# Performance work log

Measured on AMD Instinct MI355X. Metric: run time of the kernel, lower is better.

Reference implementation:

```python
import jax, jax.numpy as jnp
import numpy as np


def setup_inputs() -> dict:
    key = jax.random.key(0)
    k0, k1, k2, k3, k4 = jax.random.split(key, 5)
    dim, b, h, w = 256, 32, 56, 56
    x = jax.random.normal(k0, (b, dim, h, w), jnp.float32)
    # 1x1 conv qk: weight [out=dim, in=dim], bias [dim]
    qk_w = jax.random.normal(k1, (dim, dim), jnp.float32) * (1.0 / np.sqrt(dim))
    qk_b = jax.random.normal(k2, (dim,), jnp.float32) * 0.01
    # depthwise 3x3 conv pe: weight [dim, 1, 3, 3], bias [dim]
    pe_w = jax.random.normal(k3, (dim, 1, 3, 3), jnp.float32) * (1.0 / 3.0)
    pe_b = jax.random.normal(k4, (dim,), jnp.float32) * 0.01
    return {"x": x, "qk_w": qk_w, "qk_b": qk_b, "pe_w": pe_w, "pe_b": pe_b}


def reference(x, qk_w, qk_b, pe_w, pe_b):
    b, c, h, w = x.shape
    n = h * w
    d = c // 2                      # head_dim = dim // 2
    s = float(n) ** -0.5
    # 1x1 conv + (elu + 1) feature map
    qk = jnp.einsum('bchw,oc->bohw', x, qk_w) + qk_b[None, :, None, None]
    qk = jax.nn.elu(qk) + 1.0
    qk = qk.reshape(b, 2, d, n)
    q, k = qk[:, 0], qk[:, 1]       # each [b, d, n]
    v = x.reshape(b, c, n)          # [b, c, n]
    # kv outer product: (k*s) @ (v^T * s) -> [b, d, c]
    kv = jnp.einsum('bdn,bcn->bdc', k, v) * (s * s)
    # numerator q^T @ kv -> [b, n, c]
    num = jnp.einsum('bdn,bdc->bnc', q, kv)
    # denominator q^T @ mean(k, axis=-1) -> [b, n, 1]
    den = jnp.einsum('bdn,bd->bn', q, jnp.mean(k, axis=-1))[:, :, None] + 1e-6
    attn = (num / den).transpose(0, 2, 1).reshape(b, c, h, w)
    # depthwise 3x3 positional conv on v (= x)
    pe = jax.lax.conv_general_dilated(
        x, pe_w, window_strides=(1, 1), padding='SAME',
        dimension_numbers=('NCHW', 'OIHW', 'NCHW'), feature_group_count=c)
    return attn + pe + pe_b[None, :, None, None]
```

## Files before the change

### kernel.cpp

```cpp
#include <hip/hip_runtime.h>

#define B_ 32
#define C_ 256
#define D_ 128
#define HH 56
#define WW 56
#define N_ 3136
#define KSPLIT 14
#define KRANGE 224

typedef float f32x4 __attribute__((ext_vector_type(4)));
typedef short s16x8 __attribute__((ext_vector_type(8)));
typedef unsigned short u16x8 __attribute__((ext_vector_type(8)));

__device__ __forceinline__ int swz4(int r){
  return (r & 3) ^ (((r >> 2) & 1) << 1) ^ ((r >> 3) & 1);
}
__device__ __forceinline__ unsigned short f2bf(float f){
  unsigned u = __float_as_uint(f);
  u += 0x7fffu + ((u >> 16) & 1u);
  return (unsigned short)(u >> 16);
}
__device__ __forceinline__ float bf2f(unsigned short h){
  return __uint_as_float(((unsigned)h) << 16);
}
__device__ __forceinline__ float elu1(float v){
  return v > 0.f ? v + 1.f : __expf(v);
}
__device__ __forceinline__ unsigned cvtpk(float lo, float hi){
  unsigned r;
  asm("v_cvt_pk_bf16_f32 %0, %1, %2" : "=v"(r) : "v"(lo), "v"(hi));
  return r;
}

template<int R>
__device__ __forceinline__ void stage_glds(const unsigned short* gp, int ld, char* lds){
  const int tid = threadIdx.x;
  const int wid = tid >> 6;
#pragma unroll
  for (int q = 0; q < R/64; ++q){
    const int slot = q*256 + tid;
    const int r = slot >> 2, gi = slot & 3;
    const int u = gi ^ swz4(r);
    const unsigned short* ga = gp + r*ld + u*8;
    char* lb = lds + (q*256 + wid*64)*16;
    __builtin_amdgcn_global_load_lds(
        (__attribute__((address_space(1))) void*)ga,
        (__attribute__((address_space(3))) void*)lb, 16, 0, 0);
  }
}

__device__ __forceinline__ s16x8 ldsfrag(const char* lds, int r, int g){
  return *(const s16x8*)(lds + r*64 + ((g ^ swz4(r)) << 4));
}

__global__ __launch_bounds__(256) void k0_w(
    const float* __restrict__ w, unsigned short* __restrict__ wb)
{
  const int i = blockIdx.x*256 + threadIdx.x;
  float4 v = *(const float4*)(w + (size_t)i*4);
  uint2 h = {cvtpk(v.x, v.y), cvtpk(v.z, v.w)};
  *(uint2*)(wb + (size_t)i*4) = h;
}

__global__ __launch_bounds__(256) void k0_t(
    const float* __restrict__ x, unsigned short* __restrict__ xt)
{
  __shared__ float T[64][65];
  const int tid = threadIdx.x;
  const int n0 = blockIdx.x*64, c0 = blockIdx.y*64, b = blockIdx.z;
  const float* xb = x + ((size_t)b*C_ + c0)*N_ + n0;
#pragma unroll
  for (int q = 0; q < 4; ++q){
    const int cr = q*16 + (tid >> 4), nc = (tid & 15)*4;
    float4 v = *(const float4*)(xb + (size_t)cr*N_ + nc);
    T[cr][nc+0] = v.x; T[cr][nc+1] = v.y; T[cr][nc+2] = v.z; T[cr][nc+3] = v.w;
  }
  __syncthreads();
  const int nn = tid >> 2, cq = tid & 3;
  unsigned h[8];
#pragma unroll
  for (int j = 0; j < 8; ++j)
    h[j] = cvtpk(T[cq*16 + 2*j][nn], T[cq*16 + 2*j + 1][nn]);
  unsigned short* dst = xt + ((size_t)b*N_ + n0 + nn)*C_ + c0 + cq*16;
  *(uint4*)dst       = (uint4){h[0], h[1], h[2], h[3]};
  *(uint4*)(dst + 8) = (uint4){h[4], h[5], h[6], h[7]};
}

__global__ __launch_bounds__(256) void k1_qk(
    const unsigned short* __restrict__ xt, const unsigned short* __restrict__ wb,
    const float* __restrict__ bias,
    unsigned short* __restrict__ kbuf, unsigned short* __restrict__ qt)
{
  __shared__ __align__(16) char Al[256*64];
  __shared__ __align__(16) char Bl[64*64];
  const int tid = threadIdx.x, lane = tid & 63, wid = tid >> 6;
  const int n0 = blockIdx.x * 64;
  const int b  = blockIdx.y;
  const unsigned short* xtb = xt + ((size_t)b*N_ + n0)*C_;
  const int wo = wid*64;
  f32x4 acc[4][4] = {};

  for (int k0 = 0; k0 < C_; k0 += 32){
    __syncthreads();
    stage_glds<256>(wb + k0, C_, Al);
    stage_glds<64>(xtb + k0, C_, Bl);
    __syncthreads();
    s16x8 af[4], bv4[4];
#pragma unroll
    for (int m = 0; m < 4; ++m)  af[m]  = ldsfrag(Al, wo + m*16 + (lane & 15), lane >> 4);
#pragma unroll
    for (int nf = 0; nf < 4; ++nf) bv4[nf] = ldsfrag(Bl, nf*16 + (lane & 15), lane >> 4);
#pragma unroll
    for (int m = 0; m < 4; ++m)
#pragma unroll
      for (int nf = 0; nf < 4; ++nf)
        acc[m][nf] = __builtin_amdgcn_mfma_f32_16x16x32_bf16(af[m], bv4[nf], acc[m][nf], 0, 0, 0);
  }

  const int col = lane & 15, rg = lane >> 4;
  if (wid < 2){
#pragma unroll
    for (int m = 0; m < 4; ++m){
      const int db = wo + m*16 + rg*4;
      const float b0 = bias[db], b1 = bias[db+1], b2 = bias[db+2], b3 = bias[db+3];
#pragma unroll
      for (int nf = 0; nf < 4; ++nf){
        const int n = n0 + nf*16 + col;
        f32x4 a = acc[m][nf];
        uint2 hv = {cvtpk(elu1(a[0]+b0), elu1(a[1]+b1)),
                    cvtpk(elu1(a[2]+b2), elu1(a[3]+b3))};
        *(uint2*)(qt + ((size_t)b*N_ + n)*D_ + db) = hv;
      }
    }
  } else {
#pragma unroll
    for (int m = 0; m < 4; ++m)
#pragma unroll
      for (int j = 0; j < 4; ++j){
        const int d = wo - 128 + m*16 + rg*4 + j;
        const float bb = bias[128 + d];
#pragma unroll
        for (int nf = 0; nf < 4; ++nf){
          const int n = n0 + nf*16 + col;
          kbuf[((size_t)b*D_ + d)*N_ + n] = f2bf(elu1(acc[m][nf][j] + bb));
        }
      }
  }
}

__global__ __launch_bounds__(256) void k2_kv(
    const unsigned short* __restrict__ kbuf, const float* __restrict__ x,
    unsigned short* __restrict__ kvp, float* __restrict__ kmp)
{
  __shared__ __align__(16) char Al[128*64];
  __shared__ __align__(16) char Bl[256*64];
  const int tid = threadIdx.x, lane = tid & 63, wid = tid >> 6;
  const int ks = blockIdx.x;
  const int b  = blockIdx.y;
  const unsigned short* kb = kbuf + (size_t)b*D_*N_ + ks*KRANGE;
  const float* xb = x + (size_t)b*C_*N_ + ks*KRANGE;
  const int wd = (wid >> 1)*64, wc = (wid & 1)*128;
  f32x4 acc[4][8] = {};
  float kms = 0.f;

  for (int t = 0; t < KRANGE/32; ++t){
    __syncthreads();
    stage_glds<128>(kb + t*32, N_, Al);
#pragma unroll
    for (int q = 0; q < 8; ++q){
      int idx = q*256 + tid;
      int cc = idx >> 3, n4 = (idx & 7)*4;
      float4 v = *(const float4*)(xb + (size_t)cc*N_ + t*32 + n4);
      uint2 h = {cvtpk(v.x, v.y), cvtpk(v.z, v.w)};
      *(uint2*)(Bl + cc*64 + ((n4*2) ^ (swz4(cc) << 4))) = h;
    }
    __syncthreads();
    s16x8 af[4], bv[8];
#pragma unroll
    for (int m = 0; m < 4; ++m)  af[m] = ldsfrag(Al, wd + m*16 + (lane & 15), lane >> 4);
#pragma unroll
    for (int cf = 0; cf < 8; ++cf) bv[cf] = ldsfrag(Bl, wc + cf*16 + (lane & 15), lane >> 4);
#pragma unroll
    for (int m = 0; m < 4; ++m)
#pragma unroll
      for (int cf = 0; cf < 8; ++cf)
        acc[m][cf] = __builtin_amdgcn_mfma_f32_16x16x32_bf16(af[m], bv[cf], acc[m][cf], 0, 0, 0);
    {
      const int dr = tid >> 1, half = tid & 1;
      const char* base = Al + dr*64;
      const int s = swz4(dr);
      uint4 u0 = *(const uint4*)(base + (((half*2 + 0) ^ s) << 4));
      uint4 u1 = *(const uint4*)(base + (((half*2 + 1) ^ s) << 4));
      const unsigned ua[8] = {u0.x,u0.y,u0.z,u0.w,u1.x,u1.y,u1.z,u1.w};
#pragma unroll
      for (int i = 0; i < 8; ++i){
        kms += bf2f((unsigned short)(ua[i] & 0xffffu));
        kms += bf2f((unsigned short)(ua[i] >> 16));
      }
    }
  }

  kms += __shfl_xor(kms, 1);
  if ((tid & 1) == 0) kmp[((size_t)b*KSPLIT + ks)*D_ + (tid >> 1)] = kms;

  const int col = lane & 15, rg = lane >> 4;
#pragma unroll
  for (int m = 0; m < 4; ++m)
#pragma unroll
    for (int j = 0; j < 4; ++j){
      const int d = wd + m*16 + rg*4 + j;
#pragma unroll
      for (int cf = 0; cf < 8; ++cf){
        const int c = wc + cf*16 + col;
        kvp[(((size_t)b*KSPLIT + ks)*D_ + d)*C_ + c] = f2bf(acc[m][cf][j]);
      }
    }
}

__global__ __launch_bounds__(256) void kr_reduce(
    const unsigned short* __restrict__ kvp, const float* __restrict__ kmp,
    unsigned short* __restrict__ kvt, float* __restrict__ km)
{
  __shared__ float T[64][65];
  const int tid = threadIdx.x;
  const int ct = blockIdx.x, dt = blockIdx.y, b = blockIdx.z;
  const int d0 = dt*64, c0 = ct*64;
  const int r = tid >> 2, cq = (tid & 3)*16;
  float v[16] = {};
  for (int j = 0; j < KSPLIT; ++j){
    const unsigned short* p = kvp + (((size_t)b*KSPLIT + j)*D_ + d0 + r)*C_ + c0 + cq;
#pragma unroll
    for (int i = 0; i < 16; ++i) v[i] += bf2f(p[i]);
  }
  const float sc = 1.0f/(float)N_;
#pragma unroll
  for (int i = 0; i < 16; ++i) T[r][cq + i] = v[i]*sc;
  __syncthreads();
  u16x8 h0, h1;
#pragma unroll
  for (int i = 0; i < 8; ++i) h0[i] = f2bf(T[cq + i][r]);
#pragma unroll
  for (int i = 0; i < 8; ++i) h1[i] = f2bf(T[cq + 8 + i][r]);
  unsigned short* o = kvt + ((size_t)b*C_ + c0 + r)*D_ + d0 + cq;
  *(u16x8*)o = h0;
  *(u16x8*)(o + 8) = h1;
  if (ct == 0 && dt == 0 && tid < D_){
    float s = 0.f;
    for (int j = 0; j < KSPLIT; ++j) s += kmp[((size_t)b*KSPLIT + j)*D_ + tid];
    km[b*D_ + tid] = s*sc;
  }
}

__global__ __launch_bounds__(256) void k3_attn(
    const unsigned short* __restrict__ qt, const unsigned short* __restrict__ kvt,
    const float* __restrict__ km, unsigned short* __restrict__ attn)
{
  __shared__ __align__(16) char SM[128*72*2];
  char* Al = SM;
  char* Bl = SM + 128*64;
  unsigned short* P = (unsigned short*)SM;
  __shared__ float kms[128];
  __shared__ float dens[64];
  const int tid = threadIdx.x, lane = tid & 63, wid = tid >> 6;
  const int n0 = blockIdx.x * 64;
  const int c0 = blockIdx.y * 128;
  const int b  = blockIdx.z;
  if (tid < 128) kms[tid] = km[b*D_ + tid];
  const unsigned short* kvb = kvt + ((size_t)b*C_ + c0)*D_;
  const unsigned short* qtb = qt + ((size_t)b*N_ + n0)*D_;
  const int wc = (wid >> 1)*64, wn = (wid & 1)*32;
  f32x4 acc[4][2] = {};
  float den = 0.f;

  for (int k0 = 0; k0 < D_; k0 += 32){
    __syncthreads();
    stage_glds<128>(kvb + k0, D_, Al);
    stage_glds<64>(qtb + k0, D_, Bl);
    __syncthreads();
    s16x8 af[4], bv4[2];
#pragma unroll
    for (int m = 0; m < 4; ++m)  af[m]  = ldsfrag(Al, wc + m*16 + (lane & 15), lane >> 4);
#pragma unroll
    for (int nf = 0; nf < 2; ++nf) bv4[nf] = ldsfrag(Bl, wn + nf*16 + (lane & 15), lane >> 4);
#pragma unroll
    for (int m = 0; m < 4; ++m)
#pragma unroll
      for (int nf = 0; nf < 2; ++nf)
        acc[m][nf] = __builtin_amdgcn_mfma_f32_16x16x32_bf16(af[m], bv4[nf], acc[m][nf], 0, 0, 0);
    {
      const int nr = tid >> 2, g = tid & 3;
      uint4 u = *(const uint4*)(Bl + nr*64 + ((g ^ swz4(nr)) << 4));
      const float* kp = kms + k0 + g*8;
      const unsigned ua[4] = {u.x, u.y, u.z, u.w};
#pragma unroll
      for (int i = 0; i < 4; ++i){
        den += bf2f((unsigned short)(ua[i] & 0xffffu)) * kp[i*2];
        den += bf2f((unsigned short)(ua[i] >> 16))     * kp[i*2 + 1];
      }
    }
  }
  den += __shfl_xor(den, 1);
  den += __shfl_xor(den, 2);
  if ((tid & 3) == 0) dens[tid >> 2] = den;
  __syncthreads();

  const int col = lane & 15, rg = lane >> 4;
  float rdv[2];
#pragma unroll
  for (int nf = 0; nf < 2; ++nf)
    rdv[nf] = 1.0f / (dens[wn + nf*16 + col] + 1e-6f);
#pragma unroll
  for (int m = 0; m < 4; ++m)
#pragma unroll
    for (int nf = 0; nf < 2; ++nf)
#pragma unroll
      for (int j = 0; j < 4; ++j)
        P[(wc + m*16 + rg*4 + j)*72 + (wn + nf*16 + col)] = f2bf(acc[m][nf][j] * rdv[nf]);
  __syncthreads();

#pragma unroll
  for (int p = 0; p < 4; ++p){
    const int c = (tid >> 3) + p*32, ch = tid & 7;
    u16x8 v = *(const u16x8*)(P + c*72 + ch*8);
    *(u16x8*)(attn + ((size_t)b*C_ + c0 + c)*N_ + n0 + ch*8) = v;
  }
}

__global__ __launch_bounds__(256) void k4_pe(
    const float* __restrict__ x, const unsigned short* __restrict__ attn,
    const float* __restrict__ pw, const float* __restrict__ pb,
    float* __restrict__ out)
{
  __shared__ float xs[N_];
  const int ch = blockIdx.x, b = blockIdx.y;
  const float* xp = x + ((size_t)b*C_ + ch)*N_;
  for (int i = threadIdx.x; i < N_/4; i += 256)
    ((float4*)xs)[i] = ((const float4*)xp)[i];
  const float* wp = pw + ch*9;
  const float w00=wp[0], w01=wp[1], w02=wp[2];
  const float w10=wp[3], w11=wp[4], w12=wp[5];
  const float w20=wp[6], w21=wp[7], w22=wp[8];
  const float bias = pb[ch];
  __syncthreads();
  const unsigned short* ap = attn + ((size_t)b*C_ + ch)*N_;
  float* op = out + ((size_t)b*C_ + ch)*N_;
  for (int i = threadIdx.x; i < N_; i += 256) {
    const int hh = i / WW, ww = i - hh*WW;
    float s = bias;
    if (hh > 0) {
      const float* rp = &xs[(hh-1)*WW];
      if (ww > 0)      s += w00 * rp[ww-1];
                       s += w01 * rp[ww];
      if (ww < WW-1)   s += w02 * rp[ww+1];
    }
    {
      const float* rp = &xs[hh*WW];
      if (ww > 0)      s += w10 * rp[ww-1];
                       s += w11 * rp[ww];
      if (ww < WW-1)   s += w12 * rp[ww+1];
    }
    if (hh < HH-1) {
      const float* rp = &xs[(hh+1)*WW];
      if (ww > 0)      s += w20 * rp[ww-1];
                       s += w21 * rp[ww];
      if (ww < WW-1)   s += w22 * rp[ww+1];
    }
    op[i] = bf2f(ap[i]) + s;
  }
}

extern "C" void kernel_launch(void* const* d_in, const int* in_sizes, int n_in,
                              void* d_out, int out_size, void* d_ws, size_t ws_size,
                              hipStream_t stream) {
  (void)in_sizes; (void)n_in; (void)out_size; (void)ws_size;
  const float* x   = (const float*)d_in[0];
  const float* qkw = (const float*)d_in[1];
  const float* qkb = (const float*)d_in[2];
  const float* pew = (const float*)d_in[3];
  const float* peb = (const float*)d_in[4];
  float* out = (float*)d_out;

  unsigned short* xts  = (unsigned short*)d_ws;
  unsigned short* kbuf = xts + (size_t)B_*N_*C_;
  unsigned short* qt   = kbuf + (size_t)B_*D_*N_;
  unsigned short* kvt  = qt   + (size_t)B_*N_*D_;
  float* km  = (float*)(kvt + (size_t)B_*C_*D_);
  unsigned short* wb   = kvt;
  unsigned short* kvp  = xts;
  float* kmp = (float*)(kvp + (size_t)B_*KSPLIT*D_*C_);
  unsigned short* attn = xts;

  k0_w     <<<dim3(64),                 256, 0, stream>>>(qkw, wb);
  k0_t     <<<dim3(N_/64, C_/64, B_),   256, 0, stream>>>(x, xts);
  k1_qk    <<<dim3(N_/64, B_),          256, 0, stream>>>(xts, wb, qkb, kbuf, qt);
  k2_kv    <<<dim3(KSPLIT, B_),         256, 0, stream>>>(kbuf, x, kvp, kmp);
  kr_reduce<<<dim3(4, 2, B_),           256, 0, stream>>>(kvp, kmp, kvt, km);
  k3_attn  <<<dim3(N_/64, 2, B_),       256, 0, stream>>>(qt, kvt, km, attn);
  k4_pe    <<<dim3(C_, B_),             256, 0, stream>>>(x, attn, pew, peb, out);
}
```

Before: 186.7 us.

## Widen attn tile to all channels, vectorize depthwise conv, halve kv split

The attention kernel now computes all 256 channels per block instead of splitting channels across two blocks. This stops the denominator and q tile from being recomputed and reloaded twice, at the cost of more accumulators per wave and fewer blocks. The positional-encoding conv is rewritten with zero-padded rows in shared memory and four outputs per thread using float4 loads and stores, which removes the per-pixel branches and divisions. KSPLIT is halved, giving fewer partial kv sums to reduce but less parallelism in the kv kernel.

```diff
diff --git a/kernel.cpp b/kernel.cpp
--- a/kernel.cpp
+++ b/kernel.cpp
@@ -6,8 +6,8 @@
 #define HH 56
 #define WW 56
 #define N_ 3136
-#define KSPLIT 14
-#define KRANGE 224
+#define KSPLIT 7
+#define KRANGE 448
 
 typedef float f32x4 __attribute__((ext_vector_type(4)));
 typedef short s16x8 __attribute__((ext_vector_type(8)));
@@ -256,37 +256,36 @@
     const unsigned short* __restrict__ qt, const unsigned short* __restrict__ kvt,
     const float* __restrict__ km, unsigned short* __restrict__ attn)
 {
-  __shared__ __align__(16) char SM[128*72*2];
+  __shared__ __align__(16) char SM[256*64 + 64*64];
   char* Al = SM;
-  char* Bl = SM + 128*64;
+  char* Bl = SM + 256*64;
   unsigned short* P = (unsigned short*)SM;
   __shared__ float kms[128];
   __shared__ float dens[64];
   const int tid = threadIdx.x, lane = tid & 63, wid = tid >> 6;
   const int n0 = blockIdx.x * 64;
-  const int c0 = blockIdx.y * 128;
-  const int b  = blockIdx.z;
+  const int b  = blockIdx.y;
   if (tid < 128) kms[tid] = km[b*D_ + tid];
-  const unsigned short* kvb = kvt + ((size_t)b*C_ + c0)*D_;
+  const unsigned short* kvb = kvt + (size_t)b*C_*D_;
   const unsigned short* qtb = qt + ((size_t)b*N_ + n0)*D_;
-  const int wc = (wid >> 1)*64, wn = (wid & 1)*32;
-  f32x4 acc[4][2] = {};
+  const int wc = wid*64;
+  f32x4 acc[4][4] = {};
   float den = 0.f;
 
   for (int k0 = 0; k0 < D_; k0 += 32){
     __syncthreads();
-    stage_glds<128>(kvb + k0, D_, Al);
+    stage_glds<256>(kvb + k0, D_, Al);
     stage_glds<64>(qtb + k0, D_, Bl);
     __syncthreads();
-    s16x8 af[4], bv4[2];
+    s16x8 af[4], bv4[4];
 #pragma unroll
     for (int m = 0; m < 4; ++m)  af[m]  = ldsfrag(Al, wc + m*16 + (lane & 15), lane >> 4);
 #pragma unroll
-    for (int nf = 0; nf < 2; ++nf) bv4[nf] = ldsfrag(Bl, wn + nf*16 + (lane & 15), lane >> 4);
+    for (int nf = 0; nf < 4; ++nf) bv4[nf] = ldsfrag(Bl, nf*16 + (lane & 15), lane >> 4);
 #pragma unroll
     for (int m = 0; m < 4; ++m)
 #pragma unroll
-      for (int nf = 0; nf < 2; ++nf)
+      for (int nf = 0; nf < 4; ++nf)
         acc[m][nf] = __builtin_amdgcn_mfma_f32_16x16x32_bf16(af[m], bv4[nf], acc[m][nf], 0, 0, 0);
     {
       const int nr = tid >> 2, g = tid & 3;
@@ -306,24 +305,31 @@
   __syncthreads();
 
   const int col = lane & 15, rg = lane >> 4;
-  float rdv[2];
-#pragma unroll
-  for (int nf = 0; nf < 2; ++nf)
-    rdv[nf] = 1.0f / (dens[wn + nf*16 + col] + 1e-6f);
-#pragma unroll
-  for (int m = 0; m < 4; ++m)
-#pragma unroll
-    for (int nf = 0; nf < 2; ++nf)
-#pragma unroll
-      for (int j = 0; j < 4; ++j)
-        P[(wc + m*16 + rg*4 + j)*72 + (wn + nf*16 + col)] = f2bf(acc[m][nf][j] * rdv[nf]);
-  __syncthreads();
-
-#pragma unroll
-  for (int p = 0; p < 4; ++p){
-    const int c = (tid >> 3) + p*32, ch = tid & 7;
-    u16x8 v = *(const u16x8*)(P + c*72 + ch*8);
-    *(u16x8*)(attn + ((size_t)b*C_ + c0 + c)*N_ + n0 + ch*8) = v;
+  float rdv[4];
+#pragma unroll
+  for (int nf = 0; nf < 4; ++nf)
+    rdv[nf] = 1.0f / (dens[nf*16 + col] + 1e-6f);
+
+#pragma unroll
+  for (int h = 0; h < 2; ++h){
+    if ((wid >> 1) == h){
+      const int lc = wc - h*128;
+#pragma unroll
+      for (int m = 0; m < 4; ++m)
+#pragma unroll
+        for (int nf = 0; nf < 4; ++nf)
+#pragma unroll
+          for (int j = 0; j < 4; ++j)
+            P[(lc + m*16 + rg*4 + j)*72 + (nf*16 + col)] = f2bf(acc[m][nf][j] * rdv[nf]);
+    }
+    __syncthreads();
+#pragma unroll
+    for (int p = 0; p < 4; ++p){
+      const int c = (tid >> 3) + p*32, ch = tid & 7;
+      u16x8 v = *(const u16x8*)(P + c*72 + ch*8);
+      *(u16x8*)(attn + ((size_t)b*C_ + h*128 + c)*N_ + n0 + ch*8) = v;
+    }
+    __syncthreads();
   }
 }
 
@@ -332,41 +338,41 @@
     const float* __restrict__ pw, const float* __restrict__ pb,
     float* __restrict__ out)
 {
-  __shared__ float xs[N_];
+  __shared__ float xs_raw[58*56 + 8];
+  float* xs = xs_raw + 4;
+  const int tid = threadIdx.x;
   const int ch = blockIdx.x, b = blockIdx.y;
   const float* xp = x + ((size_t)b*C_ + ch)*N_;
-  for (int i = threadIdx.x; i < N_/4; i += 256)
-    ((float4*)xs)[i] = ((const float4*)xp)[i];
+  if (tid < 14)      ((float4*)xs)[tid] = (float4){0.f,0.f,0.f,0.f};
+  else if (tid < 28) ((float4*)xs)[784 + tid] = (float4){0.f,0.f,0.f,0.f};
+  for (int i = tid; i < 784; i += 256)
+    ((float4*)xs)[14 + i] = ((const float4*)xp)[i];
   const float* wp = pw + ch*9;
-  const float w00=wp[0], w01=wp[1], w02=wp[2];
-  const float w10=wp[3], w11=wp[4], w12=wp[5];
-  const float w20=wp[6], w21=wp[7], w22=wp[8];
+  float wgt[9];
+#pragma unroll
+  for (int i = 0; i < 9; ++i) wgt[i] = wp[i];
   const float bias = pb[ch];
   __syncthreads();
   const unsigned short* ap = attn + ((size_t)b*C_ + ch)*N_;
   float* op = out + ((size_t)b*C_ + ch)*N_;
-  for (int i = threadIdx.x; i < N_; i += 256) {
-    const int hh = i / WW, ww = i - hh*WW;
-    float s = bias;
-    if (hh > 0) {
-      const float* rp = &xs[(hh-1)*WW];
-      if (ww > 0)      s += w00 * rp[ww-1];
-                       s += w01 * rp[ww];
-      if (ww < WW-1)   s += w02 * rp[ww+1];
-    }
-    {
-      const float* rp = &xs[hh*WW];
-      if (ww > 0)      s += w10 * rp[ww-1];
-                       s += w11 * rp[ww];
-      if (ww < WW-1)   s += w12 * rp[ww+1];
-    }
-    if (hh < HH-1) {
-      const float* rp = &xs[(hh+1)*WW];
-      if (ww > 0)      s += w20 * rp[ww-1];
-                       s += w21 * rp[ww];
-      if (ww < WW-1)   s += w22 * rp[ww+1];
-    }
-    op[i] = bf2f(ap[i]) + s;
+  for (int u = tid; u < 784; u += 256) {
+    const int row = u / 14, g = u - row*14;
+    float o0 = bias, o1 = bias, o2 = bias, o3 = bias;
+#pragma unroll
+    for (int rr = 0; rr < 3; ++rr){
+      const float* rp = xs + (row + rr)*56 + g*4;
+      float4 cv = *(const float4*)rp;
+      float lf = (g > 0)  ? rp[-1] : 0.f;
+      float rt = (g < 13) ? rp[4]  : 0.f;
+      const float wl = wgt[rr*3], wc_ = wgt[rr*3+1], wr = wgt[rr*3+2];
+      o0 += wl*lf   + wc_*cv.x + wr*cv.y;
+      o1 += wl*cv.x + wc_*cv.y + wr*cv.z;
+      o2 += wl*cv.y + wc_*cv.z + wr*cv.w;
+      o3 += wl*cv.z + wc_*cv.w + wr*rt;
+    }
+    ushort4 av = *(const ushort4*)(ap + u*4);
+    float4 ov = {o0 + bf2f(av.x), o1 + bf2f(av.y), o2 + bf2f(av.z), o3 + bf2f(av.w)};
+    *(float4*)(op + u*4) = ov;
   }
 }
 
@@ -396,6 +402,6 @@
   k1_qk    <<<dim3(N_/64, B_),          256, 0, stream>>>(xts, wb, qkb, kbuf, qt);
   k2_kv    <<<dim3(KSPLIT, B_),         256, 0, stream>>>(kbuf, x, kvp, kmp);
   kr_reduce<<<dim3(4, 2, B_),           256, 0, stream>>>(kvp, kmp, kvt, km);
-  k3_attn  <<<dim3(N_/64, 2, B_),       256, 0, stream>>>(qt, kvt, km, attn);
+  k3_attn  <<<dim3(N_/64, B_),          256, 0, stream>>>(qt, kvt, km, attn);
   k4_pe    <<<dim3(C_, B_),             256, 0, stream>>>(x, attn, pew, peb, out);
 }
```

New measurement: 172.5 us. 1.08x faster.
